# Kernel tuning notes

Measured on AMD Instinct MI355X. Metric: run time of the kernel, lower is better.

## Reference

```python
import jax, jax.numpy as jnp
import numpy as np

INPUT_SIZE = 128
OUTPUT_SIZE = 32
LIFTING_DIM = 512
BATCH = 32768


def setup_inputs() -> dict:
    key = jax.random.key(0)
    ks = jax.random.split(key, 7)
    x = jax.random.normal(ks[0], (BATCH, INPUT_SIZE), dtype=jnp.float32)
    # Linear(input_size, lifting_dim) with bias (torch layout: W [out, in])
    lim1 = 1.0 / np.sqrt(INPUT_SIZE)
    W1 = jax.random.uniform(ks[1], (LIFTING_DIM, INPUT_SIZE), jnp.float32, -lim1, lim1)
    b1 = jax.random.uniform(ks[2], (LIFTING_DIM,), jnp.float32, -lim1, lim1)
    # Linear(lifting_dim, output_size, bias=False)
    lim2 = 1.0 / np.sqrt(LIFTING_DIM)
    W2 = jax.random.uniform(ks[3], (OUTPUT_SIZE, LIFTING_DIM), jnp.float32, -lim2, lim2)
    # Quadratic params: L_vars ~ randn, b ~ randn, c ~ randn (as in module init)
    n_tril = LIFTING_DIM * (LIFTING_DIM + 1) // 2
    L_vars = jax.random.normal(ks[4], (n_tril,), dtype=jnp.float32)
    qb = jax.random.normal(ks[5], (LIFTING_DIM,), dtype=jnp.float32)
    qc = jax.random.normal(ks[6], (1,), dtype=jnp.float32)
    return {"x": x, "W1": W1, "b1": b1, "W2": W2, "L_vars": L_vars, "qb": qb, "qc": qc}


def reference(x, W1, b1, W2, L_vars, qb, qc):
    # lifting: phi = tanh(x @ W1^T + b1)   [B, lifting_dim]
    phi = jnp.tanh(x @ W1.T + b1)
    # actor: linear feedback (no bias)     [B, output_size]
    pi = phi @ W2.T
    # critic: quadratic form y = phi' Q phi + b' phi + c with Q = L L^T (PSD)
    rows, cols = jnp.tril_indices(LIFTING_DIM)  # row-major, same order as torch.tril_indices
    L = jnp.zeros((LIFTING_DIM, LIFTING_DIM), dtype=L_vars.dtype).at[rows, cols].set(L_vars)
    Q = L @ L.T
    # diag(phi @ Q @ phi.T) == sum((phi @ Q) * phi, axis=1)  -- O(B*d^2), same math
    y = jnp.sum((phi @ Q) * phi, axis=1) + phi @ qb + qc  # [B]
    vf = y[:, None]  # [B, 1]
    return pi, vf
```

## Files before the change

### kernel.cpp

```cpp
#include <hip/hip_runtime.h>
#include <hip/hip_bf16.h>
#include <stdint.h>

typedef short bf16x8 __attribute__((ext_vector_type(8)));
typedef float f32x4 __attribute__((ext_vector_type(4)));

#define DEVI static __device__ __forceinline__

constexpr int B_   = 32768;
constexpr int IN_  = 128;
constexpr int LF_  = 512;
constexpr int OUT_ = 32;

constexpr size_t OFF_LTF = 0;
constexpr size_t OFF_W1F = 524288;
constexpr size_t OFF_W2F = OFF_W1F + 131072;

DEVI short f2bs(float f) { __hip_bfloat16 h = __float2bfloat16(f); return *(short*)&h; }

DEVI float tanh_fast(float v) {
    float e = __expf(2.0f * v);
    return 1.0f - 2.0f * __builtin_amdgcn_rcpf(e + 1.0f);
}

DEVI bf16x8 fragGL(const __hip_bfloat16* base, int chunk, int ln) {
    return *(const bf16x8*)(base + ((size_t)chunk * 64 + ln) * 8);
}

DEVI bf16x8 phiFrag(const char* p, int row, int kofs) {
    int c = (kofs >> 3) ^ (row & 7);
    return *(const bf16x8*)(p + (size_t)((row << 6) + c) * 16);
}
DEVI void phiStore(char* p, int row, int col, float v) {
    int c = (col >> 3) ^ (row & 7);
    *(short*)(p + (size_t)((row << 6) + c) * 16 + (col & 7) * 2) = f2bs(v);
}
DEVI bf16x8 xFrag(const char* p, int row, int kofs) {
    int c = (kofs >> 3) ^ (row & 15);
    return *(const bf16x8*)(p + (size_t)((row << 4) + c) * 16);
}

__global__ __launch_bounds__(256) void k_prep(
        const float* __restrict__ w1, const float* __restrict__ w2,
        const float* __restrict__ lv, const float* __restrict__ qb,
        __hip_bfloat16* __restrict__ w1f, __hip_bfloat16* __restrict__ w2f,
        __hip_bfloat16* __restrict__ ltf) {
    int cid = blockIdx.x * 256 + threadIdx.x;
    if (cid < 8192) {
        int ln = cid & 63, ks = (cid >> 6) & 3, nt = cid >> 8;
        int n = nt * 16 + (ln & 15), kb = ks * 32 + (ln >> 4) * 8;
        const float* src = w1 + (size_t)n * IN_ + kb;
        bf16x8 o;
#pragma unroll
        for (int i = 0; i < 8; ++i) o[i] = f2bs(src[i]);
        *(bf16x8*)(w1f + (size_t)cid * 8) = o;
    } else if (cid < 11264) {
        int c2 = cid - 8192;
        int ln = c2 & 63, ks = (c2 >> 6) & 15, nt = c2 >> 10;
        int n = nt * 16 + (ln & 15), kb = ks * 32 + (ln >> 4) * 8;
        bf16x8 o;
#pragma unroll
        for (int i = 0; i < 8; ++i) {
            float v = (n < OUT_) ? w2[(size_t)n * LF_ + kb + i]
                                 : (n == OUT_ ? qb[kb + i] : 0.f);
            o[i] = f2bs(v);
        }
        *(bf16x8*)(w2f + (size_t)c2 * 8) = o;
    } else if (cid < 44032) {
        int c3 = cid - 11264;
        int ln = c3 & 63, ks = (c3 >> 6) & 15, t = c3 >> 10;
        int j = t * 16 + (ln & 15), kb = ks * 32 + (ln >> 4) * 8;
        bf16x8 o;
#pragma unroll
        for (int i = 0; i < 8; ++i) {
            int k = kb + i;
            o[i] = (k >= j) ? f2bs(lv[(size_t)k * (k + 1) / 2 + j]) : (short)0;
        }
        *(bf16x8*)(ltf + (size_t)c3 * 8) = o;
    }
}

__global__ __launch_bounds__(512, 4) void k_fused(
        const float* __restrict__ x, const __hip_bfloat16* __restrict__ w1f,
        const float* __restrict__ b1, const __hip_bfloat16* __restrict__ w2f,
        const __hip_bfloat16* __restrict__ ltf, const float* __restrict__ qcp,
        float* __restrict__ pi, float* __restrict__ vf) {
    __shared__ char smem[40960];
    char*  phiB  = smem;
    char*  stage = smem + 32768;
    float* vfb   = (float*)stage;
    float* vfp   = (float*)(stage + 256);

    const int tid = threadIdx.x, wv = tid >> 6, ln = tid & 63;
    const int cl = ln & 15, q = ln >> 4;
    const int m0 = blockIdx.x * 32;

    {
        int row = tid >> 4, cg = tid & 15;
        const float4* p = (const float4*)(x + (size_t)(m0 + row) * IN_ + cg * 8);
        float4 u0 = p[0], u1 = p[1];
        bf16x8 pk;
        pk[0] = f2bs(u0.x); pk[1] = f2bs(u0.y); pk[2] = f2bs(u0.z); pk[3] = f2bs(u0.w);
        pk[4] = f2bs(u1.x); pk[5] = f2bs(u1.y); pk[6] = f2bs(u1.z); pk[7] = f2bs(u1.w);
        *(bf16x8*)(stage + (size_t)((row << 4) + (cg ^ (row & 15))) * 16) = pk;
    }
    __syncthreads();

    {
        f32x4 acc[2][4] = {};
#pragma unroll
        for (int ks = 0; ks < 4; ++ks) {
            bf16x8 a[2], bfr[4];
#pragma unroll
            for (int mi = 0; mi < 2; ++mi) a[mi] = xFrag(stage, mi * 16 + cl, ks * 32 + q * 8);
#pragma unroll
            for (int ni = 0; ni < 4; ++ni)
                bfr[ni] = fragGL(w1f, (4 * wv + ni) * 4 + ks, ln);
#pragma unroll
            for (int mi = 0; mi < 2; ++mi)
#pragma unroll
                for (int ni = 0; ni < 4; ++ni)
                    acc[mi][ni] = __builtin_amdgcn_mfma_f32_16x16x32_bf16(
                        a[mi], bfr[ni], acc[mi][ni], 0, 0, 0);
        }
#pragma unroll
        for (int ni = 0; ni < 4; ++ni) {
            int colg = wv * 64 + ni * 16 + cl;
            float bv = b1[colg];
#pragma unroll
            for (int mi = 0; mi < 2; ++mi)
#pragma unroll
                for (int r = 0; r < 4; ++r)
                    phiStore(phiB, mi * 16 + q * 4 + r, colg,
                             tanh_fast(acc[mi][ni][r] + bv));
        }
    }
    __syncthreads();

    if (wv < 6) {
        int mi = wv & 1, ni = wv >> 1;
        f32x4 a2a = {}, a2b = {};
#pragma unroll
        for (int ks = 0; ks < 16; ks += 2) {
            bf16x8 ae = phiFrag(phiB, mi * 16 + cl, ks * 32 + q * 8);
            bf16x8 be = fragGL(w2f, ni * 16 + ks, ln);
            a2a = __builtin_amdgcn_mfma_f32_16x16x32_bf16(ae, be, a2a, 0, 0, 0);
            bf16x8 ao = phiFrag(phiB, mi * 16 + cl, (ks + 1) * 32 + q * 8);
            bf16x8 bo = fragGL(w2f, ni * 16 + ks + 1, ln);
            a2b = __builtin_amdgcn_mfma_f32_16x16x32_bf16(ao, bo, a2b, 0, 0, 0);
        }
        f32x4 a2 = a2a + a2b;
#pragma unroll
        for (int r = 0; r < 4; ++r) {
            int row = mi * 16 + q * 4 + r, col = ni * 16 + cl;
            if (col < OUT_)       pi[(size_t)(m0 + row) * OUT_ + col] = a2[r];
            else if (col == OUT_) vfb[row] = a2[r];
        }
    }

    {
        int tl[4] = { wv, 15 - wv, 16 + wv, 31 - wv };
        int kstart[4];
#pragma unroll
        for (int j = 0; j < 4; ++j) kstart[j] = (tl[j] * 16) & ~31;
        int kmin = kstart[0];
        f32x4 acc[4][2] = {};
        bf16x8 bcur[4];
#pragma unroll
        for (int j = 0; j < 4; ++j)
            bcur[j] = fragGL(ltf, tl[j] * 16 + (kmin >> 5), ln);
        for (int k0 = kmin; k0 < LF_; k0 += 32) {
            bf16x8 a0 = phiFrag(phiB, cl,      k0 + q * 8);
            bf16x8 a1 = phiFrag(phiB, 16 + cl, k0 + q * 8);
            int kf = (k0 + 32 < LF_) ? (k0 + 32) : k0;
            bf16x8 bnx[4];
#pragma unroll
            for (int j = 0; j < 4; ++j)
                bnx[j] = fragGL(ltf, tl[j] * 16 + (kf >> 5), ln);
#pragma unroll
            for (int j = 0; j < 4; ++j) {
                if (k0 >= kstart[j]) {
                    acc[j][0] = __builtin_amdgcn_mfma_f32_16x16x32_bf16(
                        a0, bcur[j], acc[j][0], 0, 0, 0);
                    acc[j][1] = __builtin_amdgcn_mfma_f32_16x16x32_bf16(
                        a1, bcur[j], acc[j][1], 0, 0, 0);
                }
            }
#pragma unroll
            for (int j = 0; j < 4; ++j) bcur[j] = bnx[j];
        }
        float vacc[2][4];
#pragma unroll
        for (int mi = 0; mi < 2; ++mi)
#pragma unroll
            for (int r = 0; r < 4; ++r) {
                float s = 0.f;
#pragma unroll
                for (int j = 0; j < 4; ++j) { float t = acc[j][mi][r]; s += t * t; }
                s += __shfl_xor(s, 1, 64);
                s += __shfl_xor(s, 2, 64);
                s += __shfl_xor(s, 4, 64);
                s += __shfl_xor(s, 8, 64);
                vacc[mi][r] = s;
            }
        if (cl == 0)
#pragma unroll
            for (int mi = 0; mi < 2; ++mi)
#pragma unroll
                for (int r = 0; r < 4; ++r)
                    vfp[wv * 32 + mi * 16 + q * 4 + r] = vacc[mi][r];
    }
    __syncthreads();
    if (tid < 32) {
        float v = vfb[tid] + qcp[0];
#pragma unroll
        for (int w = 0; w < 8; ++w) v += vfp[w * 32 + tid];
        vf[m0 + tid] = v;
    }
}

extern "C" void kernel_launch(void* const* d_in, const int* in_sizes, int n_in,
                              void* d_out, int out_size, void* d_ws, size_t ws_size,
                              hipStream_t stream) {
    const float* x  = (const float*)d_in[0];
    const float* w1 = (const float*)d_in[1];
    const float* b1 = (const float*)d_in[2];
    const float* w2 = (const float*)d_in[3];
    const float* lv = (const float*)d_in[4];
    const float* qb = (const float*)d_in[5];
    const float* qc = (const float*)d_in[6];

    char* ws = (char*)d_ws;
    __hip_bfloat16* ltf = (__hip_bfloat16*)(ws + OFF_LTF);
    __hip_bfloat16* w1f = (__hip_bfloat16*)(ws + OFF_W1F);
    __hip_bfloat16* w2f = (__hip_bfloat16*)(ws + OFF_W2F);

    float* pi = (float*)d_out;
    float* vf = pi + (size_t)B_ * OUT_;

    k_prep <<<172, 256, 0, stream>>>(w1, w2, lv, qb, w1f, w2f, ltf);
    k_fused<<<B_ / 32, 512, 0, stream>>>(x, w1f, b1, w2f, ltf, qc, pi, vf);
}
```

Baseline: 106.9 us.

## Double fused kernel row tile to 64 rows to halve weight fragment traffic

Each block now processes 64 batch rows instead of 32, so every W1, W2 and L fragment fetched from global/L2 feeds four MFMA row tiles instead of two. The actor GEMM work is redistributed so four waves each compute two output tiles and the rest compute the critic-bias column. The explicit one-step prefetch of L fragments is dropped in favour of loading them inside the loop. LDS per block doubles to 80 KB, which lowers the number of resident blocks per CU and may reduce latency hiding.

Measured after the change: 108.1 us. Within noise of the previous version (+1.2%).

```diff
diff --git a/kernel.cpp b/kernel.cpp
--- a/kernel.cpp
+++ b/kernel.cpp
@@ -85,18 +85,19 @@
         const float* __restrict__ b1, const __hip_bfloat16* __restrict__ w2f,
         const __hip_bfloat16* __restrict__ ltf, const float* __restrict__ qcp,
         float* __restrict__ pi, float* __restrict__ vf) {
-    __shared__ char smem[40960];
+    __shared__ char smem[81920];
     char*  phiB  = smem;
-    char*  stage = smem + 32768;
+    char*  stage = smem + 65536;
     float* vfb   = (float*)stage;
     float* vfp   = (float*)(stage + 256);
 
     const int tid = threadIdx.x, wv = tid >> 6, ln = tid & 63;
     const int cl = ln & 15, q = ln >> 4;
-    const int m0 = blockIdx.x * 32;
-
-    {
-        int row = tid >> 4, cg = tid & 15;
+    const int m0 = blockIdx.x * 64;
+
+#pragma unroll
+    for (int it = 0; it < 2; ++it) {
+        int slot = it * 512 + tid, row = slot >> 4, cg = slot & 15;
         const float4* p = (const float4*)(x + (size_t)(m0 + row) * IN_ + cg * 8);
         float4 u0 = p[0], u1 = p[1];
         bf16x8 pk;
@@ -107,28 +108,27 @@
     __syncthreads();
 
     {
-        f32x4 acc[2][4] = {};
+        f32x4 acc[4][4] = {};
 #pragma unroll
         for (int ks = 0; ks < 4; ++ks) {
-            bf16x8 a[2], bfr[4];
-#pragma unroll
-            for (int mi = 0; mi < 2; ++mi) a[mi] = xFrag(stage, mi * 16 + cl, ks * 32 + q * 8);
-#pragma unroll
-            for (int ni = 0; ni < 4; ++ni)
-                bfr[ni] = fragGL(w1f, (4 * wv + ni) * 4 + ks, ln);
-#pragma unroll
-            for (int mi = 0; mi < 2; ++mi)
-#pragma unroll
-                for (int ni = 0; ni < 4; ++ni)
+            bf16x8 a[4];
+#pragma unroll
+            for (int mi = 0; mi < 4; ++mi) a[mi] = xFrag(stage, mi * 16 + cl, ks * 32 + q * 8);
+#pragma unroll
+            for (int ni = 0; ni < 4; ++ni) {
+                bf16x8 b = fragGL(w1f, (4 * wv + ni) * 4 + ks, ln);
+#pragma unroll
+                for (int mi = 0; mi < 4; ++mi)
                     acc[mi][ni] = __builtin_amdgcn_mfma_f32_16x16x32_bf16(
-                        a[mi], bfr[ni], acc[mi][ni], 0, 0, 0);
+                        a[mi], b, acc[mi][ni], 0, 0, 0);
+            }
         }
 #pragma unroll
         for (int ni = 0; ni < 4; ++ni) {
             int colg = wv * 64 + ni * 16 + cl;
             float bv = b1[colg];
 #pragma unroll
-            for (int mi = 0; mi < 2; ++mi)
+            for (int mi = 0; mi < 4; ++mi)
 #pragma unroll
                 for (int r = 0; r < 4; ++r)
                     phiStore(phiB, mi * 16 + q * 4 + r, colg,
@@ -137,17 +137,37 @@
     }
     __syncthreads();
 
-    if (wv < 6) {
-        int mi = wv & 1, ni = wv >> 1;
+    if (wv < 4) {
+        int mi0 = (2 * wv) & 3, ni0 = (2 * wv) >> 2;
+        int mi1 = (2 * wv + 1) & 3, ni1 = (2 * wv + 1) >> 2;
+        f32x4 a20 = {}, a21 = {};
+#pragma unroll 4
+        for (int ks = 0; ks < 16; ++ks) {
+            bf16x8 p0 = phiFrag(phiB, mi0 * 16 + cl, ks * 32 + q * 8);
+            bf16x8 b0 = fragGL(w2f, ni0 * 16 + ks, ln);
+            a20 = __builtin_amdgcn_mfma_f32_16x16x32_bf16(p0, b0, a20, 0, 0, 0);
+            bf16x8 p1 = phiFrag(phiB, mi1 * 16 + cl, ks * 32 + q * 8);
+            bf16x8 b1f = fragGL(w2f, ni1 * 16 + ks, ln);
+            a21 = __builtin_amdgcn_mfma_f32_16x16x32_bf16(p1, b1f, a21, 0, 0, 0);
+        }
+#pragma unroll
+        for (int r = 0; r < 4; ++r) {
+            int row0 = mi0 * 16 + q * 4 + r, col0 = ni0 * 16 + cl;
+            if (col0 < OUT_) pi[(size_t)(m0 + row0) * OUT_ + col0] = a20[r];
+            int row1 = mi1 * 16 + q * 4 + r, col1 = ni1 * 16 + cl;
+            if (col1 < OUT_) pi[(size_t)(m0 + row1) * OUT_ + col1] = a21[r];
+        }
+    } else {
+        int mi = wv - 4, ni = 2;
         f32x4 a2a = {}, a2b = {};
 #pragma unroll
         for (int ks = 0; ks < 16; ks += 2) {
-            bf16x8 ae = phiFrag(phiB, mi * 16 + cl, ks * 32 + q * 8);
+            bf16x8 pe = phiFrag(phiB, mi * 16 + cl, ks * 32 + q * 8);
             bf16x8 be = fragGL(w2f, ni * 16 + ks, ln);
-            a2a = __builtin_amdgcn_mfma_f32_16x16x32_bf16(ae, be, a2a, 0, 0, 0);
-            bf16x8 ao = phiFrag(phiB, mi * 16 + cl, (ks + 1) * 32 + q * 8);
+            a2a = __builtin_amdgcn_mfma_f32_16x16x32_bf16(pe, be, a2a, 0, 0, 0);
+            bf16x8 po = phiFrag(phiB, mi * 16 + cl, (ks + 1) * 32 + q * 8);
             bf16x8 bo = fragGL(w2f, ni * 16 + ks + 1, ln);
-            a2b = __builtin_amdgcn_mfma_f32_16x16x32_bf16(ao, bo, a2b, 0, 0, 0);
+            a2b = __builtin_amdgcn_mfma_f32_16x16x32_bf16(po, bo, a2b, 0, 0, 0);
         }
         f32x4 a2 = a2a + a2b;
 #pragma unroll
@@ -164,34 +184,26 @@
 #pragma unroll
         for (int j = 0; j < 4; ++j) kstart[j] = (tl[j] * 16) & ~31;
         int kmin = kstart[0];
-        f32x4 acc[4][2] = {};
-        bf16x8 bcur[4];
-#pragma unroll
-        for (int j = 0; j < 4; ++j)
-            bcur[j] = fragGL(ltf, tl[j] * 16 + (kmin >> 5), ln);
+        f32x4 acc[4][4] = {};
         for (int k0 = kmin; k0 < LF_; k0 += 32) {
-            bf16x8 a0 = phiFrag(phiB, cl,      k0 + q * 8);
-            bf16x8 a1 = phiFrag(phiB, 16 + cl, k0 + q * 8);
-            int kf = (k0 + 32 < LF_) ? (k0 + 32) : k0;
-            bf16x8 bnx[4];
-#pragma unroll
-            for (int j = 0; j < 4; ++j)
-                bnx[j] = fragGL(ltf, tl[j] * 16 + (kf >> 5), ln);
+            int ks = k0 >> 5;
+            bf16x8 a[4];
+#pragma unroll
+            for (int mi = 0; mi < 4; ++mi) a[mi] = phiFrag(phiB, mi * 16 + cl, k0 + q * 8);
 #pragma unroll
             for (int j = 0; j < 4; ++j) {
                 if (k0 >= kstart[j]) {
-                    acc[j][0] = __builtin_amdgcn_mfma_f32_16x16x32_bf16(
-                        a0, bcur[j], acc[j][0], 0, 0, 0);
-                    acc[j][1] = __builtin_amdgcn_mfma_f32_16x16x32_bf16(
-                        a1, bcur[j], acc[j][1], 0, 0, 0);
+                    bf16x8 b = fragGL(ltf, tl[j] * 16 + ks, ln);
+#pragma unroll
+                    for (int mi = 0; mi < 4; ++mi)
+                        acc[j][mi] = __builtin_amdgcn_mfma_f32_16x16x32_bf16(
+                            a[mi], b, acc[j][mi], 0, 0, 0);
                 }
             }
-#pragma unroll
-            for (int j = 0; j < 4; ++j) bcur[j] = bnx[j];
-        }
-        float vacc[2][4];
-#pragma unroll
-        for (int mi = 0; mi < 2; ++mi)
+        }
+        float vacc[4][4];
+#pragma unroll
+        for (int mi = 0; mi < 4; ++mi)
 #pragma unroll
             for (int r = 0; r < 4; ++r) {
                 float s = 0.f;
@@ -205,16 +217,16 @@
             }
         if (cl == 0)
 #pragma unroll
-            for (int mi = 0; mi < 2; ++mi)
+            for (int mi = 0; mi < 4; ++mi)
 #pragma unroll
                 for (int r = 0; r < 4; ++r)
-                    vfp[wv * 32 + mi * 16 + q * 4 + r] = vacc[mi][r];
+                    vfp[wv * 64 + mi * 16 + q * 4 + r] = vacc[mi][r];
     }
     __syncthreads();
-    if (tid < 32) {
+    if (tid < 64) {
         float v = vfb[tid] + qcp[0];
 #pragma unroll
-        for (int w = 0; w < 8; ++w) v += vfp[w * 32 + tid];
+        for (int w = 0; w < 8; ++w) v += vfp[w * 64 + tid];
         vf[m0 + tid] = v;
     }
 }
@@ -239,5 +251,5 @@
     float* vf = pi + (size_t)B_ * OUT_;
 
     k_prep <<<172, 256, 0, stream>>>(w1, w2, lv, qb, w1f, w2f, ltf);
-    k_fused<<<B_ / 32, 512, 0, stream>>>(x, w1f, b1, w2f, ltf, qc, pi, vf);
-}
+    k_fused<<<B_ / 64, 512, 0, stream>>>(x, w1f, b1, w2f, ltf, qc, pi, vf);
+}
```
